# Performance work log

Hardware: AMD Instinct MI355X
Metric: run time of the kernel (lower is better)

Reference implementation:

```python
import jax, jax.numpy as jnp
import numpy as np

N_NODES = 50000
N_EDGES = 800000
IN_DIM = 128
OUT_DIM = 64


def setup_inputs() -> dict:
    key = jax.random.key(0)
    k1, k2, k3, k4, k5 = jax.random.split(key, 5)
    h = jax.random.normal(k1, (N_NODES, IN_DIM), dtype=jnp.float32)
    # Xavier-normal-ish scale for weights
    W_w = jax.random.normal(k2, (IN_DIM, OUT_DIM), dtype=jnp.float32) * (2.0 / (IN_DIM + OUT_DIM)) ** 0.5
    W_b = jnp.zeros((OUT_DIM,), dtype=jnp.float32)
    A_w = jax.random.normal(k3, (2 * OUT_DIM, 1), dtype=jnp.float32) * (2.0 / (2 * OUT_DIM + 1)) ** 0.5
    A_b = jnp.zeros((1,), dtype=jnp.float32)
    src = jax.random.randint(k4, (N_EDGES,), 0, N_NODES, dtype=jnp.int32)
    dst = jax.random.randint(k5, (N_EDGES,), 0, N_NODES, dtype=jnp.int32)
    return {"h": h, "W_w": W_w, "W_b": W_b, "A_w": A_w, "A_b": A_b, "src": src, "dst": dst}


def reference(h, W_w, W_b, A_w, A_b, src, dst):
    n = h.shape[0]
    # Node projection: Wh = W(h)
    Wh = h @ W_w + W_b  # [N, D]
    # Attention logit e_ij = LeakyReLU(A([Wh_i; Wh_j])), computed as node-level
    # partial scores gathered per edge (same math as concat-linear, far less traffic).
    a_dst = (Wh @ A_w[:OUT_DIM, 0])  # [N] -> contribution of Wh_i (dst)
    a_src = (Wh @ A_w[OUT_DIM:, 0])  # [N] -> contribution of Wh_j (src)
    e = jax.nn.leaky_relu(a_dst[dst] + a_src[src] + A_b[0], negative_slope=0.2)  # [E]
    # Segment softmax over incoming edges of each destination node (stable).
    m = jax.ops.segment_max(e, dst, num_segments=n)  # [N], -inf for isolated nodes
    m = jnp.where(jnp.isfinite(m), m, 0.0)
    ex = jnp.exp(e - m[dst])  # [E]
    den = jax.ops.segment_sum(ex, dst, num_segments=n)  # [N]
    alpha = ex / den[dst]  # [E]
    # Weighted scatter-sum aggregate: h_i = sum_j alpha_ij * Wh_j
    out = jax.ops.segment_sum(alpha[:, None] * Wh[src], dst, num_segments=n)  # [N, D]
    # Dropout (p=0.6) is identity in eval mode; omitted for determinism.
    return out
```

## Files before the change

### kernel.cpp

```cpp
#include <hip/hip_runtime.h>
#include <hip/hip_bf16.h>
#include <hip/hip_fp16.h>

#define IN_DIM 128
#define OUT_DIM 64
#define MAXDEG 64

typedef __attribute__((ext_vector_type(8))) short short8v;
typedef __attribute__((ext_vector_type(4))) float float4v;
typedef unsigned short ushort_t;
typedef unsigned int uint_t;

__device__ inline ushort_t f_to_bf16(float f) {
    uint_t x = __float_as_uint(f);
    uint_t r = (x + 0x7fffu + ((x >> 16) & 1u)) >> 16;
    return (ushort_t)r;
}

__global__ __launch_bounds__(256) void gat_fused(
    const float* __restrict__ h, const float* __restrict__ W,
    const float* __restrict__ Wb, const float* __restrict__ Aw,
    ushort_t* __restrict__ Whb, float* __restrict__ a_dst_arr,
    float* __restrict__ a_src_arr, int N,
    const int* __restrict__ src, const int* __restrict__ dst,
    int* __restrict__ cnt, uint_t* __restrict__ csr, int E, int HB)
{
    __shared__ ushort_t Wl[16 * 64 * 8];

    const int t = threadIdx.x;

    if ((int)blockIdx.x < HB) {
        int base = ((int)blockIdx.x * 256 + t) * 4;
        if (base + 4 <= E) {
            int4 d4 = *(const int4*)&dst[base];
            int4 s4 = *(const int4*)&src[base];
            int r0 = atomicAdd(&cnt[d4.x], 1);
            int r1 = atomicAdd(&cnt[d4.y], 1);
            int r2 = atomicAdd(&cnt[d4.z], 1);
            int r3 = atomicAdd(&cnt[d4.w], 1);
            if (r0 < MAXDEG) csr[d4.x * MAXDEG + r0] = (uint_t)s4.x;
            if (r1 < MAXDEG) csr[d4.y * MAXDEG + r1] = (uint_t)s4.y;
            if (r2 < MAXDEG) csr[d4.z * MAXDEG + r2] = (uint_t)s4.z;
            if (r3 < MAXDEG) csr[d4.w * MAXDEG + r3] = (uint_t)s4.w;
        } else {
            for (int e = base; e < E; e++) {
                int d = dst[e];
                int r = atomicAdd(&cnt[d], 1);
                if (r < MAXDEG) csr[d * MAXDEG + r] = (uint_t)src[e];
            }
        }
        return;
    }

    const int pb = (int)blockIdx.x - HB;
    {
        int f = t * 32;
        #pragma unroll
        for (int i = 0; i < 32; i++, f++) {
            int frag = f >> 9;
            int lane = (f >> 3) & 63;
            int j    = f & 7;
            int k    = (frag >> 2) * 32 + (lane >> 4) * 8 + j;
            int d    = (frag & 3) * 16 + (lane & 15);
            Wl[f] = f_to_bf16(W[k * OUT_DIM + d]);
        }
    }
    __syncthreads();

    const int wave  = t >> 6;
    const int lane  = t & 63;
    const int node0 = (pb * 4 + wave) * 16;
    if (node0 >= N) return;
    const int quad = lane >> 4;
    const int col  = lane & 15;

    const int rowc = min(node0 + col, N - 1);
    const float* __restrict__ arow = h + (size_t)rowc * IN_DIM;

    float4v acc[4];
    #pragma unroll
    for (int db = 0; db < 4; db++) acc[db] = (float4v){0.f, 0.f, 0.f, 0.f};

    #pragma unroll
    for (int kb = 0; kb < 4; kb++) {
        const float* ap = arow + kb * 32 + quad * 8;
        float4 a0 = *(const float4*)ap;
        float4 a1 = *(const float4*)(ap + 4);
        union { short8v v; ushort_t u[8]; } af;
        af.u[0] = f_to_bf16(a0.x); af.u[1] = f_to_bf16(a0.y);
        af.u[2] = f_to_bf16(a0.z); af.u[3] = f_to_bf16(a0.w);
        af.u[4] = f_to_bf16(a1.x); af.u[5] = f_to_bf16(a1.y);
        af.u[6] = f_to_bf16(a1.z); af.u[7] = f_to_bf16(a1.w);
        #pragma unroll
        for (int db = 0; db < 4; db++) {
            short8v bf = *(const short8v*)&Wl[(((kb << 2) | db) * 64 + lane) * 8];
            acc[db] = __builtin_amdgcn_mfma_f32_16x16x32_bf16(af.v, bf, acc[db], 0, 0, 0);
        }
    }

    float wbv[4], awd[4], aws[4];
    #pragma unroll
    for (int db = 0; db < 4; db++) {
        wbv[db] = Wb[db * 16 + col];
        awd[db] = Aw[db * 16 + col];
        aws[db] = Aw[OUT_DIM + db * 16 + col];
    }

    float pd[4] = {0.f, 0.f, 0.f, 0.f};
    float ps[4] = {0.f, 0.f, 0.f, 0.f};
    #pragma unroll
    for (int db = 0; db < 4; db++) {
        #pragma unroll
        for (int r = 0; r < 4; r++) {
            float v = acc[db][r] + wbv[db];
            int node = node0 + quad * 4 + r;
            if (node < N)
                Whb[(size_t)node * OUT_DIM + db * 16 + col] = f_to_bf16(v);
            pd[r] = fmaf(v, awd[db], pd[r]);
            ps[r] = fmaf(v, aws[db], ps[r]);
        }
    }
    #pragma unroll
    for (int r = 0; r < 4; r++) {
        float d_ = pd[r], s_ = ps[r];
        #pragma unroll
        for (int off = 1; off < 16; off <<= 1) {
            d_ += __shfl_xor(d_, off);
            s_ += __shfl_xor(s_, off);
        }
        int node = node0 + quad * 4 + r;
        if (col == 0 && node < N) {
            a_dst_arr[node] = d_;
            a_src_arr[node] = s_;
        }
    }
}

__global__ __launch_bounds__(256) void gat_agg(
    const int* __restrict__ cnt, const uint_t* __restrict__ csr,
    const uint_t* __restrict__ Whb2,
    const float* __restrict__ a_dst_arr, const float* __restrict__ a_src_arr,
    const float* __restrict__ Ab,
    float* __restrict__ out, int N)
{
    int node = (int)((blockIdx.x * blockDim.x + threadIdx.x) >> 6);
    int lane = threadIdx.x & 63;
    if (node >= N) return;
    int u   = __builtin_amdgcn_readfirstlane(node);
    int deg = min(cnt[u], MAXDEG);
    float ad = a_dst_arr[u] + Ab[0];
    const uint_t* __restrict__ seg = csr + (size_t)u * MAXDEG;

    const int el = lane >> 4;
    const int dl = lane & 15;

    float ax = 0.f, ay = 0.f, az = 0.f, aw = 0.f, wsum = 0.f;

    int j = 0;
    for (; j + 16 <= deg; j += 16) {
        #pragma unroll
        for (int b = 0; b < 4; b++) {
            int   s = (int)seg[j + b * 4 + el];
            float v = ad + a_src_arr[s];
            v = (v > 0.0f) ? v : 0.2f * v;
            float w = __expf(v);
            uint2 p = *(const uint2*)&Whb2[(size_t)s * 32 + dl * 2];
            ax = fmaf(w, __uint_as_float(p.x << 16), ax);
            ay = fmaf(w, __uint_as_float(p.x & 0xffff0000u), ay);
            az = fmaf(w, __uint_as_float(p.y << 16), az);
            aw = fmaf(w, __uint_as_float(p.y & 0xffff0000u), aw);
            wsum += w;
        }
    }
    for (; j < deg; j += 4) {
        int e = j + el;
        if (e < deg) {
            int   s = (int)seg[e];
            float v = ad + a_src_arr[s];
            v = (v > 0.0f) ? v : 0.2f * v;
            float w = __expf(v);
            uint2 p = *(const uint2*)&Whb2[(size_t)s * 32 + dl * 2];
            ax = fmaf(w, __uint_as_float(p.x << 16), ax);
            ay = fmaf(w, __uint_as_float(p.x & 0xffff0000u), ay);
            az = fmaf(w, __uint_as_float(p.y << 16), az);
            aw = fmaf(w, __uint_as_float(p.y & 0xffff0000u), aw);
            wsum += w;
        }
    }

    #pragma unroll
    for (int off = 16; off < 64; off <<= 1) {
        ax   += __shfl_xor(ax, off);
        ay   += __shfl_xor(ay, off);
        az   += __shfl_xor(az, off);
        aw   += __shfl_xor(aw, off);
        wsum += __shfl_xor(wsum, off);
    }

    float inv = (deg > 0) ? 1.0f / wsum : 0.0f;
    if (lane < 16) {
        float4 o = make_float4(ax * inv, ay * inv, az * inv, aw * inv);
        *(float4*)&out[(size_t)u * OUT_DIM + dl * 4] = o;
    }
}

extern "C" void kernel_launch(void* const* d_in, const int* in_sizes, int n_in,
                              void* d_out, int out_size, void* d_ws, size_t ws_size,
                              hipStream_t stream)
{
    const float* h   = (const float*)d_in[0];
    const float* W_w = (const float*)d_in[1];
    const float* W_b = (const float*)d_in[2];
    const float* A_w = (const float*)d_in[3];
    const float* A_b = (const float*)d_in[4];
    const int*   src = (const int*)d_in[5];
    const int*   dst = (const int*)d_in[6];
    float* out = (float*)d_out;

    const int N = in_sizes[0] / IN_DIM;
    const int E = in_sizes[5];

    ushort_t* Whb   = (ushort_t*)d_ws;
    float* a_dst_a  = (float*)(Whb + (size_t)N * OUT_DIM);
    float* a_src_a  = a_dst_a + N;
    int*   cnt      = (int*)(a_src_a + N);
    uint_t* csr     = (uint_t*)(cnt + N);

    (void)hipMemsetAsync(cnt, 0, (size_t)N * sizeof(int), stream);

    {
        int HB = (E + 1023) / 1024;
        int waves = (N + 15) / 16;
        int PB = (waves + 3) / 4;
        gat_fused<<<HB + PB, 256, 0, stream>>>(h, W_w, W_b, A_w, Whb,
                                               a_dst_a, a_src_a, N,
                                               src, dst, cnt, csr, E, HB);
    }
    {
        int grid = (N + 3) / 4;
        gat_agg<<<grid, 256, 0, stream>>>(cnt, csr, (const uint_t*)Whb,
                                          a_dst_a, a_src_a, A_b, out, N);
    }
}
```

Measured before the change: 178.0 us.

## Compute attention weights once per edge lane, broadcast via shuffles in aggregation

The aggregation kernel now loads each node's neighbor list once, with one edge per lane, and computes the LeakyReLU/exp weight and the softmax normalizer with a single wave reduction. The gather loop then broadcasts source index and alpha through shuffles and has each half-wave fetch one 32-bit bf16 pair per lane, two edges at a time. This removes the per-edge exp and a_src loads that were repeated across 16 lanes in the old layout. In exchange it adds shuffle traffic, narrower 4-byte gathers per lane, and padded iterations when the degree is not a multiple of 8.

Measured after the change: 175.6 us. No clear change (-1.4%).

```diff
diff --git a/kernel.cpp b/kernel.cpp
--- a/kernel.cpp
+++ b/kernel.cpp
@@ -148,59 +148,47 @@
     if (node >= N) return;
     int u   = __builtin_amdgcn_readfirstlane(node);
     int deg = min(cnt[u], MAXDEG);
+    const uint_t* __restrict__ seg = csr + (size_t)u * MAXDEG;
+
     float ad = a_dst_arr[u] + Ab[0];
-    const uint_t* __restrict__ seg = csr + (size_t)u * MAXDEG;
-
-    const int el = lane >> 4;
-    const int dl = lane & 15;
-
-    float ax = 0.f, ay = 0.f, az = 0.f, aw = 0.f, wsum = 0.f;
-
-    int j = 0;
-    for (; j + 16 <= deg; j += 16) {
+    int   s_l = 0;
+    float w_l = 0.f;
+    if (lane < deg) {
+        s_l = (int)seg[lane];
+        float v = ad + a_src_arr[s_l];
+        v = (v > 0.0f) ? v : 0.2f * v;
+        w_l = __expf(v);
+    }
+    float ws = w_l;
+    #pragma unroll
+    for (int off = 1; off < 64; off <<= 1) ws += __shfl_xor(ws, off);
+    float inv  = (deg > 0) ? 1.0f / ws : 0.0f;
+    float al_l = w_l * inv;
+
+    const int el = lane >> 5;
+    const int dl = lane & 31;
+
+    float accx = 0.f, accy = 0.f;
+
+    for (int j = 0; j < deg; j += 8) {
         #pragma unroll
         for (int b = 0; b < 4; b++) {
-            int   s = (int)seg[j + b * 4 + el];
-            float v = ad + a_src_arr[s];
-            v = (v > 0.0f) ? v : 0.2f * v;
-            float w = __expf(v);
-            uint2 p = *(const uint2*)&Whb2[(size_t)s * 32 + dl * 2];
-            ax = fmaf(w, __uint_as_float(p.x << 16), ax);
-            ay = fmaf(w, __uint_as_float(p.x & 0xffff0000u), ay);
-            az = fmaf(w, __uint_as_float(p.y << 16), az);
-            aw = fmaf(w, __uint_as_float(p.y & 0xffff0000u), aw);
-            wsum += w;
-        }
-    }
-    for (; j < deg; j += 4) {
-        int e = j + el;
-        if (e < deg) {
-            int   s = (int)seg[e];
-            float v = ad + a_src_arr[s];
-            v = (v > 0.0f) ? v : 0.2f * v;
-            float w = __expf(v);
-            uint2 p = *(const uint2*)&Whb2[(size_t)s * 32 + dl * 2];
-            ax = fmaf(w, __uint_as_float(p.x << 16), ax);
-            ay = fmaf(w, __uint_as_float(p.x & 0xffff0000u), ay);
-            az = fmaf(w, __uint_as_float(p.y << 16), az);
-            aw = fmaf(w, __uint_as_float(p.y & 0xffff0000u), aw);
-            wsum += w;
-        }
-    }
-
-    #pragma unroll
-    for (int off = 16; off < 64; off <<= 1) {
-        ax   += __shfl_xor(ax, off);
-        ay   += __shfl_xor(ay, off);
-        az   += __shfl_xor(az, off);
-        aw   += __shfl_xor(aw, off);
-        wsum += __shfl_xor(wsum, off);
-    }
-
-    float inv = (deg > 0) ? 1.0f / wsum : 0.0f;
-    if (lane < 16) {
-        float4 o = make_float4(ax * inv, ay * inv, az * inv, aw * inv);
-        *(float4*)&out[(size_t)u * OUT_DIM + dl * 4] = o;
+            int   e  = j + b * 2 + el;
+            int   ss = __shfl(s_l, e);
+            float al = __shfl(al_l, e);
+            al = (e < deg) ? al : 0.0f;
+            uint_t p = Whb2[(size_t)ss * 32 + dl];
+            accx = fmaf(al, __uint_as_float(p << 16), accx);
+            accy = fmaf(al, __uint_as_float(p & 0xffff0000u), accy);
+        }
+    }
+
+    accx += __shfl_xor(accx, 32);
+    accy += __shfl_xor(accy, 32);
+
+    if (lane < 32) {
+        float2 o = make_float2(accx, accy);
+        *(float2*)&out[(size_t)u * OUT_DIM + dl * 2] = o;
     }
 }
 
```
